# Performance work log

Hardware: AMD Instinct MI355X
Metric: run time of the kernel (lower is better)

Reference implementation:

```python
import jax, jax.numpy as jnp
import numpy as np

B, N, D, H, NCTX = 4, 2048, 1024, 16, 512
HD = D // H  # head dim = 64


def setup_inputs() -> dict:
    key = jax.random.key(0)
    ks = jax.random.split(key, 6)
    return {
        "x": jax.random.normal(ks[0], (B, N, D), dtype=jnp.float32),
        "ctx_ppr": jax.random.uniform(ks[1], (B, NCTX), dtype=jnp.float32),
        "ctx_trust": jax.random.normal(ks[2], (B, NCTX), dtype=jnp.float32),
        "W_in": jax.random.normal(ks[3], (D, 3 * D), dtype=jnp.float32) * 0.02,
        "b_in": jnp.zeros((3 * D,), dtype=jnp.float32),
        "W_out": jax.random.normal(ks[4], (D, D), dtype=jnp.float32) * 0.02,
        "b_out": jnp.zeros((D,), dtype=jnp.float32),
        "log_ppr_alpha": jnp.full((1,), 0.1, dtype=jnp.float32),
        "trust_scale": jnp.full((1,), 0.1, dtype=jnp.float32),
        "n_ctx": NCTX,
    }


def reference(x, ctx_ppr, ctx_trust, W_in, b_in, W_out, b_out, log_ppr_alpha, trust_scale, n_ctx):
    b, n, dmodel = x.shape
    # QKV projection
    qkv = x @ W_in + b_in                                   # [B,N,3D]
    q, k, v = jnp.split(qkv, 3, axis=-1)
    q = q.reshape(b, n, H, HD).transpose(0, 2, 1, 3)        # [B,H,N,d]
    k = k.reshape(b, n, H, HD).transpose(0, 2, 1, 3)
    v = v.reshape(b, n, H, HD).transpose(0, 2, 1, 3)
    if n_ctx > 0:
        # multiplicative trust gate on context-token values
        gate = jax.nn.sigmoid(trust_scale * ctx_trust)      # [B,n_ctx]
        gate_full = jnp.concatenate(
            [gate, jnp.ones((b, n - n_ctx), dtype=x.dtype)], axis=1)  # [B,N]
        v = v * gate_full[:, None, :, None]
        # additive graph (log-PPR) column bias on attention logits
        col_bias = -log_ppr_alpha * jnp.log(jnp.maximum(ctx_ppr, 1e-8))  # [B,n_ctx]
        bias = jnp.concatenate(
            [col_bias, jnp.zeros((b, n - n_ctx), dtype=x.dtype)], axis=1)  # [B,N]
    else:
        bias = jnp.zeros((b, n), dtype=x.dtype)
    scale = 1.0 / np.sqrt(HD).astype(np.float32)
    scores = jnp.einsum("bhqd,bhkd->bhqk", q, k) * scale + bias[:, None, None, :]
    attn = jax.nn.softmax(scores, axis=-1)                  # [B,H,N,N]
    out = jnp.einsum("bhqk,bhkd->bhqd", attn, v)            # [B,H,N,d]
    out = out.transpose(0, 2, 1, 3).reshape(b, n, dmodel)
    return out @ W_out + b_out
```

## Files before the change

kernel.cpp:

```cpp
#include <hip/hip_runtime.h>
#include <hip/hip_bf16.h>
#include <stdint.h>

#define BATCH  4
#define NSEQ   2048
#define DMODEL 1024
#define NHEAD  16
#define HDIM   64
#define NCTXC  512

typedef unsigned short u16;
typedef __attribute__((ext_vector_type(8))) short bfrag;
typedef __attribute__((ext_vector_type(4))) float facc;

typedef __attribute__((address_space(3))) void lds_void;
typedef __attribute__((address_space(1))) void g_void;

__device__ __forceinline__ void gload16(const void* g, void* l) {
  __builtin_amdgcn_global_load_lds((const g_void*)g, (lds_void*)l, 16, 0, 0);
}

__device__ __forceinline__ u16 f2bf(float f) {
  uint32_t r;
  asm("v_cvt_pk_bf16_f32 %0, %1, %1" : "=v"(r) : "v"(f));
  return (u16)r;
}

#if __has_builtin(__builtin_amdgcn_cvt_pk_bf16_f32)
__device__ __forceinline__ uint32_t pk2bf(float a, float b) {
  return __builtin_bit_cast(uint32_t, __builtin_amdgcn_cvt_pk_bf16_f32(a, b));
}
#else
__device__ __forceinline__ uint32_t pk2bf(float a, float b) {
  uint32_t r;
  asm("v_cvt_pk_bf16_f32 %0, %1, %2" : "=v"(r) : "v"(a), "v"(b));
  return r;
}
#endif

__device__ __forceinline__ float bf2f(u16 h) {
  union { uint32_t u; float f; } un;
  un.u = ((uint32_t)h) << 16;
  return un.f;
}

__device__ __forceinline__ float load_flex(const void* p, size_t idx, int isb) {
  return isb ? bf2f(((const u16*)p)[idx]) : ((const float*)p)[idx];
}

__device__ __forceinline__ uint4 pack8(float4 a, float4 b) {
  uint4 r;
  r.x = pk2bf(a.x, a.y);
  r.y = pk2bf(a.z, a.w);
  r.z = pk2bf(b.x, b.y);
  r.w = pk2bf(b.z, b.w);
  return r;
}

__global__ __launch_bounds__(256) void detect_kernel(const u16* __restrict__ xraw,
                                                     int* __restrict__ flag) {
  __shared__ int s_high, s_zero;
  if (threadIdx.x == 0) { s_high = 0; s_zero = 0; }
  __syncthreads();
  int h = 0, z = 0;
  for (int i = threadIdx.x; i < 4096; i += 256) {
    const u16 v = xraw[2 * i];
    const int e = (v >> 7) & 0xFF;
    if (e >= 0x90) h++;
    if (v == 0) z++;
  }
  atomicAdd(&s_high, h);
  atomicAdd(&s_zero, z);
  __syncthreads();
  if (threadIdx.x == 0) flag[0] = (s_high < 64 && s_zero < 2048) ? 1 : 0;
}


__global__ __launch_bounds__(256) void cast_x_kernel(const void* __restrict__ x,
                                                     u16* __restrict__ xb,
                                                     const int* __restrict__ flag) {
  const int isb = flag[0];
  const int i = blockIdx.x * 256 + threadIdx.x;
  if (isb) {
    ((uint4*)xb)[i] = ((const uint4*)x)[i];
  } else {
    const float4 f0 = ((const float4*)x)[2 * i];
    const float4 f1 = ((const float4*)x)[2 * i + 1];
    ((uint4*)xb)[i] = pack8(f0, f1);
  }
}

__global__ __launch_bounds__(256) void transpose_flex(const void* __restrict__ W,
                                                      u16* __restrict__ Wt,
                                                      int R, int C,
                                                      const int* __restrict__ flag) {
  __shared__ float tile[32][33];
  const int isb = flag[0];
  const int tx = threadIdx.x;
  const int ty = threadIdx.y;
  const int c0 = blockIdx.x * 32;
  const int r0 = blockIdx.y * 32;
#pragma unroll
  for (int j = 0; j < 32; j += 8)
    tile[ty + j][tx] = load_flex(W, (size_t)(r0 + ty + j) * C + c0 + tx, isb);
  __syncthreads();
#pragma unroll
  for (int j = 0; j < 32; j += 8)
    Wt[(size_t)(c0 + ty + j) * R + r0 + tx] = f2bf(tile[tx][ty + j]);
}

__global__ __launch_bounds__(256) void prep_small(const void* __restrict__ b_in,
                                                  const void* __restrict__ b_out,
                                                  const void* __restrict__ ppr,
                                                  const void* __restrict__ trust,
                                                  const void* __restrict__ alpha_p,
                                                  const void* __restrict__ ts_p,
                                                  float* __restrict__ bin_f,
                                                  float* __restrict__ bout_f,
                                                  float* __restrict__ gate,
                                                  float* __restrict__ cbias,
                                                  const int* __restrict__ flag) {
  const int isb = flag[0];
  const int i = blockIdx.x * 256 + threadIdx.x;
  if (i < 3072) {
    bin_f[i] = load_flex(b_in, i, isb);
  } else if (i < 4096) {
    bout_f[i - 3072] = load_flex(b_out, i - 3072, isb);
  } else if (i < 4096 + BATCH * NCTXC) {
    const int j = i - 4096;
    const float ts = load_flex(ts_p, 0, isb), al = load_flex(alpha_p, 0, isb);
    gate[j]  = 1.0f / (1.0f + __expf(-ts * load_flex(trust, j, isb)));
    cbias[j] = -al * logf(fmaxf(load_flex(ppr, j, isb), 1e-8f)) * 1.44269504f;
  }
}

__device__ __forceinline__ void kloop_mfma(const u16* __restrict__ Ag,
                                           const u16* __restrict__ Bg,
                                           u16* As, u16* Bs,
                                           int tid, int wM, int wN, int l16, int quad,
                                           facc acc[4][4]) {
  char* ldsA = (char*)As + tid * 16;
  char* ldsB = (char*)Bs + tid * 16;
  for (int k0 = 0; k0 < 1024; k0 += 32) {
    __syncthreads();
    gload16(Ag + k0, ldsA);
    gload16(Ag + (size_t)64 * 1024 + k0, ldsA + 4096);
    gload16(Bg + k0, ldsB);
    gload16(Bg + (size_t)64 * 1024 + k0, ldsB + 4096);
    __syncthreads();

    bfrag af[4], bf[4];
#pragma unroll
    for (int i = 0; i < 4; ++i)
      af[i] = *(const bfrag*)(&As[(wM + i * 16 + l16) * 32 + quad * 8]);
#pragma unroll
    for (int j = 0; j < 4; ++j)
      bf[j] = *(const bfrag*)(&Bs[(wN + j * 16 + l16) * 32 + quad * 8]);
#pragma unroll
    for (int i = 0; i < 4; ++i)
#pragma unroll
      for (int j = 0; j < 4; ++j)
        acc[i][j] = __builtin_amdgcn_mfma_f32_16x16x32_bf16(af[i], bf[j], acc[i][j], 0, 0, 0);
  }
}

__global__ __launch_bounds__(256) void gemm_qkvt(const u16* __restrict__ xb,
                                                 const u16* __restrict__ Wt,
                                                 const float* __restrict__ bin_f,
                                                 const float* __restrict__ gate,
                                                 u16* __restrict__ qk,
                                                 u16* __restrict__ Vtg) {
  __shared__ u16 As[128 * 32];
  __shared__ u16 Bs[128 * 32];
  const int tid  = threadIdx.x;
  const int w    = tid >> 6;
  const int lane = tid & 63;
  const int quad = lane >> 4;
  const int l16  = lane & 15;
  const int wM   = (w >> 1) * 64;
  const int wN   = (w & 1) * 64;
  const int id   = blockIdx.x;
  const int srow  = tid >> 2;
  const int spart = tid & 3;

  facc acc[4][4] = {};

  if (id < 1024) {
    const int bn = id & 15, bm = id >> 4;
    const u16* Ag = xb + (size_t)(bm * 128 + srow) * 1024 + spart * 8;
    const u16* Bg = Wt + (size_t)(bn * 128 + srow) * 1024 + spart * 8;
    kloop_mfma(Ag, Bg, As, Bs, tid, wM, wN, l16, quad, acc);

    const float qs = (bn < 8) ? 0.18033688f : 1.0f;
#pragma unroll
    for (int i = 0; i < 4; ++i) {
      const int grow0 = bm * 128 + wM + i * 16 + quad * 4;
#pragma unroll
      for (int j = 0; j < 4; ++j) {
        const int gcol = bn * 128 + wN + j * 16 + l16;
        const float bv = bin_f[gcol];
#pragma unroll
        for (int r = 0; r < 4; ++r)
          qk[(size_t)(grow0 + r) * 2048 + gcol] = f2bf((acc[i][j][r] + bv) * qs);
      }
    }
  } else {
    const int id2 = id - 1024;
    const int bn = id2 & 63, bm = id2 >> 6;
    const u16* Ag = Wt + (size_t)2048 * 1024 + (size_t)(bm * 128 + srow) * 1024 + spart * 8;
    const u16* Bg = xb + (size_t)(bn * 128 + srow) * 1024 + spart * 8;
    kloop_mfma(Ag, Bg, As, Bs, tid, wM, wN, l16, quad, acc);

#pragma unroll
    for (int i = 0; i < 4; ++i) {
      const int grow0 = bm * 128 + wM + i * 16 + quad * 4;
      const int h   = grow0 >> 6;
      const int dd0 = grow0 & 63;
#pragma unroll
      for (int j = 0; j < 4; ++j) {
        const int gcol = bn * 128 + wN + j * 16 + l16;
        const int bb  = gcol >> 11;
        const int tok = gcol & (NSEQ - 1);
        const float gl = (tok < NCTXC) ? gate[bb * NCTXC + tok] : 1.0f;
        u16* dst = &Vtg[((size_t)((bb * NHEAD + h) * HDIM + dd0)) * NSEQ + tok];
#pragma unroll
        for (int r = 0; r < 4; ++r)
          dst[(size_t)r * NSEQ] = f2bf((acc[i][j][r] + bin_f[2 * DMODEL + grow0 + r]) * gl);
      }
    }
  }
}

__global__ __launch_bounds__(256) void gemm_out(const u16* __restrict__ A,
                                                const u16* __restrict__ Bt,
                                                const float* __restrict__ biasf,
                                                void* __restrict__ Cout,
                                                const int* __restrict__ flag) {
  __shared__ u16 As[128 * 32];
  __shared__ u16 Bs[128 * 32];
  const int isb  = flag[0];
  const int tid  = threadIdx.x;
  const int w    = tid >> 6;
  const int lane = tid & 63;
  const int quad = lane >> 4;
  const int l16  = lane & 15;
  const int wM   = (w >> 1) * 64;
  const int wN   = (w & 1) * 64;
  const int bm   = blockIdx.y;
  const int bn   = blockIdx.x;
  const int srow  = tid >> 2;
  const int spart = tid & 3;

  facc acc[4][4] = {};
  const u16* Ag = A + (size_t)(bm * 128 + srow) * 2048 + spart * 8;
  const u16* Bg = Bt + (size_t)(bn * 128 + srow) * 1024 + spart * 8;
  char* ldsA = (char*)As + tid * 16;
  char* ldsB = (char*)Bs + tid * 16;

  for (int k0 = 0; k0 < 1024; k0 += 32) {
    __syncthreads();
    gload16(Ag + k0, ldsA);
    gload16(Ag + (size_t)64 * 2048 + k0, ldsA + 4096);
    gload16(Bg + k0, ldsB);
    gload16(Bg + (size_t)64 * 1024 + k0, ldsB + 4096);
    __syncthreads();

    bfrag af[4], bf[4];
#pragma unroll
    for (int i = 0; i < 4; ++i)
      af[i] = *(const bfrag*)(&As[(wM + i * 16 + l16) * 32 + quad * 8]);
#pragma unroll
    for (int j = 0; j < 4; ++j)
      bf[j] = *(const bfrag*)(&Bs[(wN + j * 16 + l16) * 32 + quad * 8]);
#pragma unroll
    for (int i = 0; i < 4; ++i)
#pragma unroll
      for (int j = 0; j < 4; ++j)
        acc[i][j] = __builtin_amdgcn_mfma_f32_16x16x32_bf16(af[i], bf[j], acc[i][j], 0, 0, 0);
  }

#pragma unroll
  for (int i = 0; i < 4; ++i) {
    const int grow0 = bm * 128 + wM + i * 16 + quad * 4;
#pragma unroll
    for (int j = 0; j < 4; ++j) {
      const int gcol = bn * 128 + wN + j * 16 + l16;
      const float bv = biasf[gcol];
#pragma unroll
      for (int r = 0; r < 4; ++r) {
        const float v = acc[i][j][r] + bv;
        if (isb) ((u16*)Cout)[(size_t)(grow0 + r) * 1024 + gcol] = f2bf(v);
        else     ((float*)Cout)[(size_t)(grow0 + r) * 1024 + gcol] = v;
      }
    }
  }
}

__global__ __launch_bounds__(256) void attn_kernel(u16* __restrict__ qk,
                                                   const u16* __restrict__ vtg,
                                                   const float* __restrict__ cbias) {
  const int id    = blockIdx.x;
  const int chunk = id >> 3;
  const int qt    = chunk & 15;
  const int hg    = (id & 7) | ((chunk >> 4) << 3);
  const int h     = hg & 15;
  const int b     = hg >> 4;

  __shared__ u16 Ks[64 * 72];
  __shared__ u16 Vt[64 * 72];
  __shared__ u16 Ps[8][16 * 72];

  const int tid  = threadIdx.x;
  const int w    = tid >> 6;
  const int lane = tid & 63;
  const int quad = lane >> 4;
  const int l16  = lane & 15;
  const int srow = tid >> 2;
  const int spart = tid & 3;

  bfrag bq[2][2];
#pragma unroll
  for (int qs = 0; qs < 2; ++qs) {
    const u16* qrow = qk + (size_t)(b * NSEQ + qt * 128 + (w * 2 + qs) * 16 + l16) * 2048 + h * HDIM;
    bq[qs][0] = *(const bfrag*)(qrow + quad * 8);
    bq[qs][1] = *(const bfrag*)(qrow + 32 + quad * 8);
  }

  float lp[2] = {0.0f, 0.0f};
  facc o[2][4] = {};

  const u16* kst = qk + (size_t)(b * NSEQ) * 2048 + DMODEL + h * HDIM;
  const u16* vst = vtg + (size_t)((b * NHEAD + h) * HDIM + srow) * NSEQ;
  u16* psw[2] = { Ps[w * 2], Ps[w * 2 + 1] };

  uint4 pk0, pk1, pv0, pv1;
  {
    const u16* ks = kst + (size_t)srow * 2048 + spart * 16;
    pk0 = *(const uint4*)ks;
    pk1 = *(const uint4*)(ks + 8);
    const u16* vs = vst + spart * 16;
    pv0 = *(const uint4*)vs;
    pv1 = *(const uint4*)(vs + 8);
  }

  for (int t = 0; t < NSEQ / 64; ++t) {
    __syncthreads();
    *(uint4*)(&Ks[srow * 72 + spart * 16])     = pk0;
    *(uint4*)(&Ks[srow * 72 + spart * 16 + 8]) = pk1;
    *(uint4*)(&Vt[srow * 72 + spart * 16])     = pv0;
    *(uint4*)(&Vt[srow * 72 + spart * 16 + 8]) = pv1;
    __syncthreads();

    {
      const int tn = (t < NSEQ / 64 - 1) ? t + 1 : t;
      const u16* ks = kst + (size_t)(tn * 64 + srow) * 2048 + spart * 16;
      pk0 = *(const uint4*)ks;
      pk1 = *(const uint4*)(ks + 8);
      const u16* vs = vst + tn * 64 + spart * 16;
      pv0 = *(const uint4*)vs;
      pv1 = *(const uint4*)(vs + 8);
    }

    bfrag ak[4][2], av[4][2];
#pragma unroll
    for (int nt = 0; nt < 4; ++nt) {
      ak[nt][0] = *(const bfrag*)(&Ks[(nt * 16 + l16) * 72 + quad * 8]);
      ak[nt][1] = *(const bfrag*)(&Ks[(nt * 16 + l16) * 72 + 32 + quad * 8]);
      av[nt][0] = *(const bfrag*)(&Vt[(nt * 16 + l16) * 72 + quad * 8]);
      av[nt][1] = *(const bfrag*)(&Vt[(nt * 16 + l16) * 72 + 32 + quad * 8]);
    }

#pragma unroll
    for (int qs = 0; qs < 2; ++qs) {
      facc s[4];
#pragma unroll
      for (int nt = 0; nt < 4; ++nt) {
        facc z = {};
        z = __builtin_amdgcn_mfma_f32_16x16x32_bf16(ak[nt][0], bq[qs][0], z, 0, 0, 0);
        s[nt] = __builtin_amdgcn_mfma_f32_16x16x32_bf16(ak[nt][1], bq[qs][1], z, 0, 0, 0);
      }

      float rs = 0.0f;
      if (t < 8) {
        const float* cb = cbias + b * NCTXC + t * 64 + quad * 4;
#pragma unroll
        for (int nt = 0; nt < 4; ++nt)
#pragma unroll
          for (int r = 0; r < 4; ++r) {
            const float p = __builtin_amdgcn_exp2f(s[nt][r] + cb[nt * 16 + r]);
            s[nt][r] = p;
            rs += p;
          }
      } else {
#pragma unroll
        for (int nt = 0; nt < 4; ++nt)
#pragma unroll
          for (int r = 0; r < 4; ++r) {
            const float p = __builtin_amdgcn_exp2f(s[nt][r]);
            s[nt][r] = p;
            rs += p;
          }
      }
      lp[qs] += rs;

#pragma unroll
      for (int nt = 0; nt < 4; ++nt) {
        uint2 pk;
        pk.x = pk2bf(s[nt][0], s[nt][1]);
        pk.y = pk2bf(s[nt][2], s[nt][3]);
        *(uint2*)(&psw[qs][l16 * 72 + nt * 16 + quad * 4]) = pk;
      }
    }

#pragma unroll
    for (int qs = 0; qs < 2; ++qs) {
      const bfrag bp0 = *(const bfrag*)(&psw[qs][l16 * 72 + quad * 8]);
      const bfrag bp1 = *(const bfrag*)(&psw[qs][l16 * 72 + 32 + quad * 8]);
#pragma unroll
      for (int dt = 0; dt < 4; ++dt) {
        o[qs][dt] = __builtin_amdgcn_mfma_f32_16x16x32_bf16(av[dt][0], bp0, o[qs][dt], 0, 0, 0);
        o[qs][dt] = __builtin_amdgcn_mfma_f32_16x16x32_bf16(av[dt][1], bp1, o[qs][dt], 0, 0, 0);
      }
    }
  }

#pragma unroll
  for (int qs = 0; qs < 2; ++qs) {
    float l = lp[qs];
    l += __shfl_xor(l, 16);
    l += __shfl_xor(l, 32);
    const float inv = 1.0f / l;
    u16* orow = qk + (size_t)(b * NSEQ + qt * 128 + (w * 2 + qs) * 16 + l16) * 2048 + h * HDIM;
#pragma unroll
    for (int dt = 0; dt < 4; ++dt) {
      uint2 st;
      st.x = pk2bf(o[qs][dt][0] * inv, o[qs][dt][1] * inv);
      st.y = pk2bf(o[qs][dt][2] * inv, o[qs][dt][3] * inv);
      *(uint2*)(orow + dt * 16 + quad * 4) = st;
    }
  }
}


extern "C" void kernel_launch(void* const* d_in, const int* in_sizes, int n_in,
                              void* d_out, int out_size, void* d_ws, size_t ws_size,
                              hipStream_t stream) {
  const void* x          = d_in[0];
  const void* ctx_ppr    = d_in[1];
  const void* ctx_trust  = d_in[2];
  const void* W_in       = d_in[3];
  const void* b_in       = d_in[4];
  const void* W_out      = d_in[5];
  const void* b_out      = d_in[6];
  const void* lppr_alpha = d_in[7];
  const void* tscale     = d_in[8];

  char* ws = (char*)d_ws;
  u16* Wt    = (u16*)ws;  ws += (size_t)3072 * 1024 * 2;
  u16* WoT   = (u16*)ws;  ws += (size_t)1024 * 1024 * 2;
  u16* qk    = (u16*)ws;  ws += (size_t)8192 * 2048 * 2;
  u16* Vtg   = (u16*)ws;  ws += (size_t)64 * 64 * 2048 * 2;
  u16* xb    = (u16*)ws;  ws += (size_t)8192 * 1024 * 2;
  float* bin_f  = (float*)ws; ws += 3072 * 4;
  float* bout_f = (float*)ws; ws += 1024 * 4;
  float* gate   = (float*)ws; ws += (size_t)BATCH * NCTXC * 4;
  float* cbias  = (float*)ws; ws += (size_t)BATCH * NCTXC * 4;
  int*   flag   = (int*)ws;   ws += 64;

  detect_kernel<<<dim3(1), dim3(256), 0, stream>>>((const u16*)x, flag);
  cast_x_kernel<<<dim3(4096), dim3(256), 0, stream>>>(x, xb, flag);
  transpose_flex<<<dim3(96, 32), dim3(32, 8), 0, stream>>>(W_in, Wt, 1024, 3072, flag);
  transpose_flex<<<dim3(32, 32), dim3(32, 8), 0, stream>>>(W_out, WoT, 1024, 1024, flag);
  prep_small<<<dim3(24), dim3(256), 0, stream>>>(b_in, b_out, ctx_ppr, ctx_trust,
                                                 lppr_alpha, tscale,
                                                 bin_f, bout_f, gate, cbias, flag);
  gemm_qkvt<<<dim3(1536), dim3(256), 0, stream>>>(xb, Wt, bin_f, gate, qk, Vtg);
  attn_kernel<<<dim3(1024), dim3(256), 0, stream>>>(qk, Vtg, cbias);
  gemm_out<<<dim3(8, 64), dim3(256), 0, stream>>>(qk, WoT, bout_f, d_out, flag);
}
```

Baseline: 314.3 us.

## Fold bias into MFMA accumulator, compute softmax denominator via ones-MFMA, add setprio

The context column bias now seeds the QK^T MFMA accumulator instead of being added per element before exp2. The row-sum of the probabilities is computed by an extra MFMA against a ones fragment on the bf16 P tile, replacing VALU adds and the cross-lane shuffles. s_setprio hints are placed around the MFMA blocks. This takes VALU work off the softmax at the cost of two extra MFMAs per query subtile, and the denominator now sums bf16-rounded P values, which changes numerics slightly.

```diff
diff --git a/kernel.cpp b/kernel.cpp
--- a/kernel.cpp
+++ b/kernel.cpp
@@ -326,7 +326,11 @@
     bq[qs][1] = *(const bfrag*)(qrow + 32 + quad * 8);
   }
 
-  float lp[2] = {0.0f, 0.0f};
+  bfrag ones;
+#pragma unroll
+  for (int i = 0; i < 8; ++i) ones[i] = (short)0x3F80;
+
+  facc den[2] = {};
   facc o[2][4] = {};
 
   const u16* kst = qk + (size_t)(b * NSEQ) * 2048 + DMODEL + h * HDIM;
@@ -370,38 +374,33 @@
       av[nt][1] = *(const bfrag*)(&Vt[(nt * 16 + l16) * 72 + 32 + quad * 8]);
     }
 
+    facc zb[4];
+    if (t < 8) {
+      const float* cb = cbias + b * NCTXC + t * 64 + quad * 4;
+#pragma unroll
+      for (int nt = 0; nt < 4; ++nt) zb[nt] = *(const facc*)(cb + nt * 16);
+    } else {
+#pragma unroll
+      for (int nt = 0; nt < 4; ++nt) zb[nt] = (facc){};
+    }
+
 #pragma unroll
     for (int qs = 0; qs < 2; ++qs) {
       facc s[4];
+      __builtin_amdgcn_s_setprio(1);
 #pragma unroll
       for (int nt = 0; nt < 4; ++nt) {
-        facc z = {};
+        facc z = zb[nt];
         z = __builtin_amdgcn_mfma_f32_16x16x32_bf16(ak[nt][0], bq[qs][0], z, 0, 0, 0);
-        s[nt] = __builtin_amdgcn_mfma_f32_16x16x32_bf16(ak[nt][1], bq[qs][1], z, 0, 0, 0);
-      }
-
-      float rs = 0.0f;
-      if (t < 8) {
-        const float* cb = cbias + b * NCTXC + t * 64 + quad * 4;
-#pragma unroll
-        for (int nt = 0; nt < 4; ++nt)
-#pragma unroll
-          for (int r = 0; r < 4; ++r) {
-            const float p = __builtin_amdgcn_exp2f(s[nt][r] + cb[nt * 16 + r]);
-            s[nt][r] = p;
-            rs += p;
-          }
-      } else {
-#pragma unroll
-        for (int nt = 0; nt < 4; ++nt)
-#pragma unroll
-          for (int r = 0; r < 4; ++r) {
-            const float p = __builtin_amdgcn_exp2f(s[nt][r]);
-            s[nt][r] = p;
-            rs += p;
-          }
-      }
-      lp[qs] += rs;
+        s[nt] = __builtin_amdgcn_mfma_f32_16x16x32_bf16(ak[nt][1], bq[qs][1], s[nt] = z, 0, 0, 0);
+      }
+      __builtin_amdgcn_s_setprio(0);
+
+#pragma unroll
+      for (int nt = 0; nt < 4; ++nt)
+#pragma unroll
+        for (int r = 0; r < 4; ++r)
+          s[nt][r] = __builtin_amdgcn_exp2f(s[nt][r]);
 
 #pragma unroll
       for (int nt = 0; nt < 4; ++nt) {
@@ -416,20 +415,21 @@
     for (int qs = 0; qs < 2; ++qs) {
       const bfrag bp0 = *(const bfrag*)(&psw[qs][l16 * 72 + quad * 8]);
       const bfrag bp1 = *(const bfrag*)(&psw[qs][l16 * 72 + 32 + quad * 8]);
+      __builtin_amdgcn_s_setprio(1);
 #pragma unroll
       for (int dt = 0; dt < 4; ++dt) {
         o[qs][dt] = __builtin_amdgcn_mfma_f32_16x16x32_bf16(av[dt][0], bp0, o[qs][dt], 0, 0, 0);
         o[qs][dt] = __builtin_amdgcn_mfma_f32_16x16x32_bf16(av[dt][1], bp1, o[qs][dt], 0, 0, 0);
       }
+      den[qs] = __builtin_amdgcn_mfma_f32_16x16x32_bf16(ones, bp0, den[qs], 0, 0, 0);
+      den[qs] = __builtin_amdgcn_mfma_f32_16x16x32_bf16(ones, bp1, den[qs], 0, 0, 0);
+      __builtin_amdgcn_s_setprio(0);
     }
   }
 
 #pragma unroll
   for (int qs = 0; qs < 2; ++qs) {
-    float l = lp[qs];
-    l += __shfl_xor(l, 16);
-    l += __shfl_xor(l, 32);
-    const float inv = 1.0f / l;
+    const float inv = 1.0f / den[qs][0];
     u16* orow = qk + (size_t)(b * NSEQ + qt * 128 + (w * 2 + qs) * 16 + l16) * 2048 + h * HDIM;
 #pragma unroll
     for (int dt = 0; dt < 4; ++dt) {
```

Result: no change. 309.6 us (-1.5%).
